# Optimization experiments

Measured on AMD Instinct MI355X. Metric: run time of the kernel, lower is better.

The kernel has to match this reference:

```python
import jax, jax.numpy as jnp
import numpy as np

IN_CH = 512; OUT_CH = 512; NOISE_SIZE = 512; K = 3; A = 0.2
B = 4; H = 32
_G = float(np.sqrt(2.0 / (1.0 + A * A)))                 # leaky_relu gain, a=0.2
CONV_SCALE = _G / float(np.sqrt(IN_CH * K * K))          # equal-lr kaiming scale (fan_in = in_ch*3*3)
MS_SCALE = float(np.sqrt(2.0 / (NOISE_SIZE + IN_CH)))    # equal-lr xavier scale on make_s linear
RGB_SCALE = _G * float(np.sqrt(2.0 / (OUT_CH + 3)))      # equal-lr xavier scale on 1x1 to_rgb


def upsample2x(x):
    # torch F.interpolate(scale_factor=2, mode='bilinear', align_corners=False)
    b, c, h, w = x.shape
    return jax.image.resize(x, (b, c, 2 * h, 2 * w), method='bilinear')


def mod_conv(x, style, weight, bias, ms_w, ms_b, w_scale, demodulate, pad):
    # style -> per-sample input-channel scales s: (B, Cin)
    s = style @ (ms_w.T * MS_SCALE) + ms_b
    Wmod = (weight * w_scale)[None] * s[:, None, :, None, None]   # (B, Cout, Cin, k, k)
    if demodulate:
        d = jax.lax.rsqrt(jnp.sum(Wmod * Wmod, axis=(2, 3, 4)) + 1e-8)
        Wmod = Wmod * d[:, :, None, None, None]
    conv1 = lambda xi, wi: jax.lax.conv_general_dilated(
        xi[None], wi, (1, 1), [(pad, pad), (pad, pad)],
        dimension_numbers=('NCHW', 'OIHW', 'NCHW'))[0]
    y = jax.vmap(conv1)(x, Wmod)                                   # per-sample weights == grouped conv
    return y + bias[None, :, None, None]


def lrelu(x):
    return jnp.where(x >= 0, x, A * x)


def setup_inputs() -> dict:
    key = jax.random.key(0)
    ks = jax.random.split(key, 19)
    r = lambda i, shape: jax.random.normal(ks[i], shape, dtype=jnp.float32)
    return {
        'maps': r(0, (B, IN_CH, H, H)),
        'w': r(1, (B, NOISE_SIZE)),
        'rgb': r(2, (B, 3, H, H)),
        'noise0': r(3, (B, 1, 2 * H, 2 * H)),
        'noise1': r(4, (B, 1, 2 * H, 2 * H)),
        'conv0_w': r(5, (OUT_CH, IN_CH, K, K)),
        'conv0_b': 0.1 * r(6, (OUT_CH,)),
        'ms0_w': r(7, (IN_CH, NOISE_SIZE)),
        'ms0_b': jnp.ones((IN_CH,), jnp.float32),
        'ns0': 0.1 * r(8, (OUT_CH,)),
        'conv1_w': r(9, (OUT_CH, OUT_CH, K, K)),
        'conv1_b': 0.1 * r(10, (OUT_CH,)),
        'ms1_w': r(11, (OUT_CH, NOISE_SIZE)),
        'ms1_b': jnp.ones((OUT_CH,), jnp.float32),
        'ns1': 0.1 * r(12, (OUT_CH,)),
        'rgb_w': r(13, (3, OUT_CH, 1, 1)),
        'rgb_b': 0.1 * r(14, (3,)),
        'msr_w': r(15, (OUT_CH, NOISE_SIZE)),
        'msr_b': jnp.ones((OUT_CH,), jnp.float32),
    }


def reference(maps, w, rgb, noise0, noise1,
              conv0_w, conv0_b, ms0_w, ms0_b, ns0,
              conv1_w, conv1_b, ms1_w, ms1_b, ns1,
              rgb_w, rgb_b, msr_w, msr_b):
    # upsample branch (upsample=True)
    rgb = upsample2x(rgb)
    maps = upsample2x(maps)
    # layer 0: modulated conv -> noise -> leaky relu
    h = mod_conv(maps, w, conv0_w, conv0_b, ms0_w, ms0_b, CONV_SCALE, True, 1)
    h = lrelu(h + ns0[None, :, None, None] * noise0)
    # layer 1
    h = mod_conv(h, w, conv1_w, conv1_b, ms1_w, ms1_b, CONV_SCALE, True, 1)
    h = lrelu(h + ns1[None, :, None, None] * noise1)
    # to_rgb: 1x1 modulated conv, no demodulation
    rgb_out = rgb + mod_conv(h, w, rgb_w, rgb_b, msr_w, msr_b, RGB_SCALE, False, 0)
    return (rgb_out, h)
```

## Files before the change

kernel.cpp:

```cpp
#include <hip/hip_runtime.h>
#include <stdint.h>


#define BATCH 4
#define CH 512
#define NPP 4356
#define HOUT_OFF 49152

static constexpr double G_GAIN = 1.3867504905630728;
static constexpr float CONV_SCALE_F = (float)(G_GAIN / 67.88225099390857);
static constexpr float MS_SCALE_F = 0.044194173824159216f;
static constexpr float RGB_SCALE_F = (float)(G_GAIN * 1.4142135623730951 / 22.693611435820433);

typedef __attribute__((ext_vector_type(8))) short short8;
typedef __attribute__((ext_vector_type(4))) float floatx4;

#define OFF_FLAG   0
#define OFF_S0     256
#define OFF_S1     (OFF_S0 + 8192)
#define OFF_SR     (OFF_S1 + 8192)
#define OFF_D0     (OFF_SR + 8192)
#define OFF_D1     (OFF_D0 + 8192)
#define OFF_B0F    (OFF_D1 + 8192)
#define OFF_B1F    (OFF_B0F + 2048)
#define OFF_NS0F   (OFF_B1F + 2048)
#define OFF_NS1F   (OFF_NS0F + 2048)
#define OFF_RGBBF  (OFF_NS1F + 2048)
#define OFF_WMODR  (OFF_RGBBF + 256)
#define OFF_N0F    (OFF_WMODR + 24576)
#define OFF_N1F    (OFF_N0F + 65536)
#define OFF_WT0    (OFF_N1F + 65536)
#define WT_BYTES   4718592
#define OFF_WT1    (OFF_WT0 + WT_BYTES)
#define OFF_XP0    (OFF_WT1 + WT_BYTES)
#define XP_BYTES   17842176
#define OFF_XP1    (OFF_XP0 + XP_BYTES)

__device__ __forceinline__ float bf2f(unsigned short u) {
  return __uint_as_float(((unsigned int)u) << 16);
}
__device__ __forceinline__ unsigned short f2bf(float f) {
  unsigned int x = __float_as_uint(f);
  unsigned int r = x + 0x7FFFu + ((x >> 16) & 1u);
  return (unsigned short)(r >> 16);
}
__device__ __forceinline__ float ldin(const void* p, long i, int bf) {
  if (bf) return bf2f(((const unsigned short*)p)[i]);
  return ((const float*)p)[i];
}
__device__ __forceinline__ void async_ld16(const void* g, void* l) {
  __builtin_amdgcn_global_load_lds(
      (const __attribute__((address_space(1))) unsigned int*)g,
      (__attribute__((address_space(3))) unsigned int*)l, 16, 0, 0);
}
__device__ __forceinline__ void upw(int o, int n_in, int& lo, int& hi, float& wlo) {
  int k = o >> 1;
  if (o & 1) { lo = k; hi = k + 1; if (hi > n_in - 1) hi = n_in - 1; wlo = 0.75f; }
  else       { lo = k - 1; if (lo < 0) lo = 0; hi = k; wlo = 0.25f; }
}

__global__ void k_flag(const unsigned int* msb, int* flag) {
  if (threadIdx.x == 0 && blockIdx.x == 0)
    *flag = (msb[0] == 0x3F803F80u) ? 1 : 0;
}

__global__ void k_zero(unsigned short* Xp) {
  const int idx = blockIdx.x * 256 + threadIdx.x;
  const int plane = idx / 132;
  const int rem = idx - plane * 132;
  const int row65 = rem >= 66;
  const int col = rem - (row65 ? 66 : 0);
  const short8 z = {0, 0, 0, 0, 0, 0, 0, 0};
  *(short8*)&Xp[((long)plane * NPP + (row65 ? 65 : 0) * 66 + col) * 8] = z;
}

__global__ void k_styles(const void* w, const void* msw0, const void* msb0,
                         const void* msw1, const void* msb1,
                         const void* mswr, const void* msbr,
                         float* s0, float* s1, float* sr, const int* flagp) {
  const int bf = *flagp;
  const int mat = blockIdx.x >> 7, chunk = blockIdx.x & 127;
  const int wv = threadIdx.x >> 6, lane = threadIdx.x & 63;
  const int i = chunk * 4 + wv;
  const void* msw; const void* msb; float* out;
  if (mat == 0)      { msw = msw0; msb = msb0; out = s0; }
  else if (mat == 1) { msw = msw1; msb = msb1; out = s1; }
  else               { msw = mswr; msb = msbr; out = sr; }
  float a[4] = {0.f, 0.f, 0.f, 0.f};
  const int n0 = lane * 8;
  if (bf) {
    short8 m8 = *(const short8*)((const unsigned short*)msw + (long)i * 512 + n0);
    for (int b = 0; b < 4; ++b) {
      short8 w8 = *(const short8*)((const unsigned short*)w + b * 512 + n0);
      float s = 0.f;
      for (int e = 0; e < 8; ++e)
        s += bf2f((unsigned short)m8[e]) * bf2f((unsigned short)w8[e]);
      a[b] = s;
    }
  } else {
    const float* mrow = (const float*)msw + (long)i * 512 + n0;
    float4 m0v = *(const float4*)mrow, m1v = *(const float4*)(mrow + 4);
    for (int b = 0; b < 4; ++b) {
      const float* wr = (const float*)w + b * 512 + n0;
      float4 w0v = *(const float4*)wr, w1v = *(const float4*)(wr + 4);
      a[b] = m0v.x * w0v.x + m0v.y * w0v.y + m0v.z * w0v.z + m0v.w * w0v.w +
             m1v.x * w1v.x + m1v.y * w1v.y + m1v.z * w1v.z + m1v.w * w1v.w;
    }
  }
  for (int off = 1; off < 64; off <<= 1)
    for (int b = 0; b < 4; ++b) a[b] += __shfl_xor(a[b], off, 64);
  if (lane == 0) {
    const float mb = ldin(msb, i, bf);
    for (int b = 0; b < 4; ++b) out[b * 512 + i] = a[b] * MS_SCALE_F + mb;
  }
}

__global__ void k_convert(const void* b0, const void* b1, const void* nv0, const void* nv1,
                          const void* rb, const void* rw, const void* noise0, const void* noise1,
                          float* ob0, float* ob1, float* ons0, float* ons1, float* orb,
                          float* owmr, float* on0, float* on1,
                          const float* sr, const int* flagp) {
  const int bf = *flagp;
  const int t = blockIdx.x * blockDim.x + threadIdx.x;
  const int stride = gridDim.x * blockDim.x;
  if (t < 512) {
    ob0[t] = ldin(b0, t, bf); ob1[t] = ldin(b1, t, bf);
    ons0[t] = ldin(nv0, t, bf); ons1[t] = ldin(nv1, t, bf);
  }
  if (t < 3) orb[t] = ldin(rb, t, bf);
  for (int i = t; i < 16384; i += stride) {
    on0[i] = ldin(noise0, i, bf);
    on1[i] = ldin(noise1, i, bf);
  }
  for (int i = t; i < 4 * 3 * 512; i += stride) {
    int b = i / 1536; int r = i - b * 1536; int c = r >> 9; int ci = r & 511;
    owmr[i] = RGB_SCALE_F * ldin(rw, c * 512 + ci, bf) * sr[b * 512 + ci];
  }
}

__global__ void k_wtd(const void* w0, const void* w1, const float* s0, const float* s1,
                      unsigned short* Wt0, unsigned short* Wt1,
                      float* S0, float* S1, const int* flagp) {
  const int bf = *flagp;
  const int l = blockIdx.x >> 9, co = blockIdx.x & 511;
  const void* w = l ? w1 : w0;
  const float* s = l ? s1 : s0;
  unsigned short* Wt = l ? Wt1 : Wt0;
  float* S = l ? S1 : S0;
  float part[4] = {0.f, 0.f, 0.f, 0.f};
  for (int h = 0; h < 2; ++h) {
    const int ci = threadIdx.x + h * 256;
    const int kb = ci >> 5, q = (ci >> 3) & 3, j = ci & 7;
    const long rbase = ((long)co * 512 + ci) * 9;
    float wsq = 0.f;
    for (int t = 0; t < 9; ++t) {
      float v = ldin(w, rbase + t, bf);
      wsq += v * v;
      Wt[((((long)t * 16 + kb) * 4 + q) * 512 + co) * 8 + j] = f2bf(v);
    }
    for (int b = 0; b < 4; ++b) {
      float sv = s[b * 512 + ci];
      part[b] += sv * sv * wsq;
    }
  }
  __shared__ float red[256 * 4];
  for (int b = 0; b < 4; ++b) red[threadIdx.x * 4 + b] = part[b];
  __syncthreads();
  for (int off = 128; off > 0; off >>= 1) {
    if (threadIdx.x < off)
      for (int b = 0; b < 4; ++b)
        red[threadIdx.x * 4 + b] += red[(threadIdx.x + off) * 4 + b];
    __syncthreads();
  }
  if (threadIdx.x < 4) S[threadIdx.x * 512 + co] = red[threadIdx.x];
}

__global__ void k_upt(const void* maps, const float* s0, unsigned short* Xp0,
                      const int* flagp) {
  const int bf = *flagp;
  const int t = blockIdx.x, kb = blockIdx.y, b = blockIdx.z;
  __shared__ float lds[32][4][32];
  {
    const int ciq = threadIdx.x >> 5;
    const int x = threadIdx.x & 31;
    for (int cc = 0; cc < 4; ++cc) {
      const int ci = cc * 8 + ciq;
      const long cbase = ((long)(b * 512 + kb * 32 + ci)) << 10;
      for (int r = 0; r < 4; ++r) {
        int ir = 2 * t - 1 + r;
        ir = ir < 0 ? 0 : (ir > 31 ? 31 : ir);
        lds[ci][r][x] = ldin(maps, cbase + ir * 32 + x, bf);
      }
    }
  }
  __syncthreads();
  const int q = threadIdx.x >> 6, px = threadIdx.x & 63;
  int xlo, xhi; float wx;
  upw(px, 32, xlo, xhi, wx);
  float sv[8];
  for (int jj = 0; jj < 8; ++jj) sv[jj] = s0[b * 512 + kb * 32 + q * 8 + jj];
  for (int y = 0; y < 4; ++y) {
    const int yg = 4 * t + y;
    int ylo, yhi; float wy;
    upw(yg, 32, ylo, yhi, wy);
    const int rlo = ylo - (2 * t - 1), rhi = yhi - (2 * t - 1);
    short8 pk;
    for (int jj = 0; jj < 8; ++jj) {
      const int ci = q * 8 + jj;
      float vlo = wx * lds[ci][rlo][xlo] + (1.f - wx) * lds[ci][rlo][xhi];
      float vhi = wx * lds[ci][rhi][xlo] + (1.f - wx) * lds[ci][rhi][xhi];
      float v = (wy * vlo + (1.f - wy) * vhi) * sv[jj];
      pk[jj] = (short)f2bf(v);
    }
    *(short8*)&Xp0[((((long)b * 16 + kb) * 4 + q) * NPP + (yg + 1) * 66 + (px + 1)) * 8] = pk;
  }
}

#define MFMA16 __builtin_amdgcn_mfma_f32_16x16x32_bf16
template <int LAYER>
__global__ __launch_bounds__(256, 2) void k_conv(
    const unsigned short* __restrict__ Wt,
    const unsigned short* Xp,
    const float* __restrict__ Ssum,
    const float* __restrict__ bias,
    const float* __restrict__ nsc,
    const float* __restrict__ noise,
    const float* __restrict__ snext,
    unsigned short* XpOut,
    void* dout,
    const int* __restrict__ flagp) {
  __shared__ __align__(16) unsigned short Bl[8192];
  const int idx = blockIdx.x;
  const int mt = idx & 3, b = (idx >> 2) & 3, nt = idx >> 4;
  const int m0 = mt << 7, y0 = nt << 1;
  const int lane = threadIdx.x & 63, wv = threadIdx.x >> 6;
  const int wm = wv >> 1, wn = wv & 1;
  const int q = lane >> 4, l15 = lane & 15;

  const floatx4 vz = {0.f, 0.f, 0.f, 0.f};
  floatx4 c00 = vz, c01 = vz, c02 = vz, c03 = vz;
  floatx4 c10 = vz, c11 = vz, c12 = vz, c13 = vz;
  floatx4 c20 = vz, c21 = vz, c22 = vz, c23 = vz;
  floatx4 c30 = vz, c31 = vz, c32 = vz, c33 = vz;

  const unsigned short* Wbase = Wt + ((long)q * 512 + m0 + wm * 64 + l15) * 8;

  auto issueB2 = [&](int kb, int r0) {
    for (int r = 0; r < 2; ++r) {
      const int row = r0 + r;
      const unsigned short* src =
          Xp + ((((long)b * 16 + kb) * 4 + wv) * NPP + (long)(y0 + row) * 66 + 1 + lane) * 8;
      async_ld16(src, &Bl[((row * 4 + wv) * 64) * 8]);
    }
  };

  issueB2(0, 0);

  const short8 z8 = {0, 0, 0, 0, 0, 0, 0, 0};
#pragma unroll 1
  for (int kb = 0; kb < 16; ++kb) {
#pragma unroll 1
    for (int ky = 0; ky < 3; ++ky) {
      short8 a_[3][4];
#pragma unroll
      for (int kx = 0; kx < 3; ++kx) {
        const unsigned short* ap = Wbase + ((long)((ky * 3 + kx) * 16 + kb) * 4) * 512 * 8;
#pragma unroll
        for (int i = 0; i < 4; ++i)
          a_[kx][i] = *(const short8*)(ap + i * 128);
      }
      __syncthreads();
      if (ky == 0) issueB2(kb, 2);
      else if (ky == 2) issueB2(kb + 1 == 16 ? 0 : kb + 1, 0);
      const int sq = ((wn + ky) * 4 + q) * 64;
#define TAPC(KX)                                                               \
  {                                                                            \
    short8 aa0 = a_[KX][0], aa1 = a_[KX][1], aa2 = a_[KX][2], aa3 = a_[KX][3]; \
    short8 bb0, bb1, bb2, bb3;                                                 \
    {                                                                          \
      int p = 0 * 16 + l15 + (KX);                                             \
      int pc = p < 1 ? 0 : p - 1;                                              \
      bb0 = *(const short8*)&Bl[(sq + pc) * 8];                                \
      if ((KX) == 0) bb0 = (p == 0) ? z8 : bb0;                                \
    }                                                                          \
    bb1 = *(const short8*)&Bl[(sq + 1 * 16 + l15 + (KX)-1) * 8];               \
    bb2 = *(const short8*)&Bl[(sq + 2 * 16 + l15 + (KX)-1) * 8];               \
    {                                                                          \
      int p = 3 * 16 + l15 + (KX);                                             \
      int pc = p > 64 ? 63 : p - 1;                                            \
      bb3 = *(const short8*)&Bl[(sq + pc) * 8];                                \
      if ((KX) == 2) bb3 = (p == 65) ? z8 : bb3;                               \
    }                                                                          \
    c00 = MFMA16(aa0, bb0, c00, 0, 0, 0); c01 = MFMA16(aa0, bb1, c01, 0, 0, 0);\
    c02 = MFMA16(aa0, bb2, c02, 0, 0, 0); c03 = MFMA16(aa0, bb3, c03, 0, 0, 0);\
    c10 = MFMA16(aa1, bb0, c10, 0, 0, 0); c11 = MFMA16(aa1, bb1, c11, 0, 0, 0);\
    c12 = MFMA16(aa1, bb2, c12, 0, 0, 0); c13 = MFMA16(aa1, bb3, c13, 0, 0, 0);\
    c20 = MFMA16(aa2, bb0, c20, 0, 0, 0); c21 = MFMA16(aa2, bb1, c21, 0, 0, 0);\
    c22 = MFMA16(aa2, bb2, c22, 0, 0, 0); c23 = MFMA16(aa2, bb3, c23, 0, 0, 0);\
    c30 = MFMA16(aa3, bb0, c30, 0, 0, 0); c31 = MFMA16(aa3, bb1, c31, 0, 0, 0);\
    c32 = MFMA16(aa3, bb2, c32, 0, 0, 0); c33 = MFMA16(aa3, bb3, c33, 0, 0, 0);\
  }
      TAPC(0)
      TAPC(1)
      TAPC(2)
#undef TAPC
    }
  }

  floatx4 accv[4][4] = {{c00, c01, c02, c03}, {c10, c11, c12, c13},
                        {c20, c21, c22, c23}, {c30, c31, c32, c33}};
  const int bfflag = *flagp;
  const int coB = m0 + (wm << 6) + ((lane >> 4) << 2);
  const int xB = lane & 15;
  const int y = y0 + wn;
  for (int i = 0; i < 4; ++i) {
    const int co = coB + (i << 4);
    float Ds[4], bi[4], nv[4], sx[4];
    for (int r = 0; r < 4; ++r) {
      float Sv = Ssum[b * 512 + co + r];
      Ds[r] = CONV_SCALE_F * rsqrtf(CONV_SCALE_F * CONV_SCALE_F * Sv + 1e-8f);
      bi[r] = bias[co + r];
      nv[r] = nsc[co + r];
      sx[r] = (LAYER == 0) ? snext[b * 512 + co + r] : 0.f;
    }
    for (int j = 0; j < 4; ++j) {
      const int x = (j << 4) + xB;
      const int p = (y << 6) + x;
      const float nz = noise[b * 4096 + p];
      if (LAYER == 0) {
        unsigned long long pk = 0ull;
        for (int r = 0; r < 4; ++r) {
          float v = accv[i][j][r] * Ds[r] + bi[r] + nv[r] * nz;
          v = (v >= 0.f) ? v : 0.2f * v;
          pk |= (unsigned long long)f2bf(v * sx[r]) << (16 * r);
        }
        const int pp = (y + 1) * 66 + (x + 1);
        const long o = ((((long)b * 16 + (co >> 5)) * 4 + ((co >> 3) & 3)) * NPP + pp) * 8 + (co & 7);
        *(unsigned long long*)(XpOut + o) = pk;
      } else {
        for (int r = 0; r < 4; ++r) {
          float v = accv[i][j][r] * Ds[r] + bi[r] + nv[r] * nz;
          v = (v >= 0.f) ? v : 0.2f * v;
          const long o = (((long)(b * 512 + co + r)) << 12) + p;
          if (bfflag) ((unsigned short*)dout)[HOUT_OFF + o] = f2bf(v);
          else        ((float*)dout)[HOUT_OFF + o] = v;
        }
      }
    }
  }
}

__global__ void k_rgb(const void* rgb_in, const float* wmodr, const float* rgbb,
                      void* dout, const int* flagp) {
  const int bf = *flagp;
  const int b = blockIdx.y, p0 = blockIdx.x * 64;
  const int px = threadIdx.x & 63, g = threadIdx.x >> 6;
  const char* hbytes = (const char*)dout + (long)HOUT_OFF * (bf ? 2 : 4);
  float a0 = 0.f, a1 = 0.f, a2 = 0.f;
  const float* wm = wmodr + b * 1536;
  for (int ci = g * 128; ci < g * 128 + 128; ++ci) {
    const long o = (((long)(b * 512 + ci)) << 12) + p0 + px;
    const float hv = bf ? bf2f(((const unsigned short*)hbytes)[o])
                        : ((const float*)hbytes)[o];
    a0 += wm[ci] * hv;
    a1 += wm[512 + ci] * hv;
    a2 += wm[1024 + ci] * hv;
  }
  __shared__ float red[4][3][64];
  red[g][0][px] = a0; red[g][1][px] = a1; red[g][2][px] = a2;
  __syncthreads();
  if (g == 0) {
    const int p = p0 + px;
    const int y = p >> 6, x = p & 63;
    int ylo, yhi, xlo, xhi; float wy, wx;
    upw(y, 32, ylo, yhi, wy);
    upw(x, 32, xlo, xhi, wx);
    for (int c = 0; c < 3; ++c) {
      float s = red[0][c][px] + red[1][c][px] + red[2][c][px] + red[3][c][px];
      const long base = (long)(b * 3 + c) << 10;
      const float v00 = ldin(rgb_in, base + ylo * 32 + xlo, bf);
      const float v01 = ldin(rgb_in, base + ylo * 32 + xhi, bf);
      const float v10 = ldin(rgb_in, base + yhi * 32 + xlo, bf);
      const float v11 = ldin(rgb_in, base + yhi * 32 + xhi, bf);
      const float up = wy * (wx * v00 + (1.f - wx) * v01) +
                       (1.f - wy) * (wx * v10 + (1.f - wx) * v11);
      const float v = up + s + rgbb[c];
      const long o = ((long)(b * 3 + c) << 12) + p;
      if (bf) ((unsigned short*)dout)[o] = f2bf(v);
      else    ((float*)dout)[o] = v;
    }
  }
}

extern "C" void kernel_launch(void* const* d_in, const int* in_sizes, int n_in,
                              void* d_out, int out_size, void* d_ws, size_t ws_size,
                              hipStream_t stream) {
  char* ws = (char*)d_ws;
  int* flag = (int*)(ws + OFF_FLAG);
  float* s0 = (float*)(ws + OFF_S0);
  float* s1 = (float*)(ws + OFF_S1);
  float* sr = (float*)(ws + OFF_SR);
  float* S0 = (float*)(ws + OFF_D0);
  float* S1 = (float*)(ws + OFF_D1);
  float* b0f = (float*)(ws + OFF_B0F);
  float* b1f = (float*)(ws + OFF_B1F);
  float* ns0f = (float*)(ws + OFF_NS0F);
  float* ns1f = (float*)(ws + OFF_NS1F);
  float* rgbbf = (float*)(ws + OFF_RGBBF);
  float* wmodr = (float*)(ws + OFF_WMODR);
  float* n0f = (float*)(ws + OFF_N0F);
  float* n1f = (float*)(ws + OFF_N1F);
  unsigned short* Wt0 = (unsigned short*)(ws + OFF_WT0);
  unsigned short* Wt1 = (unsigned short*)(ws + OFF_WT1);
  unsigned short* Xp0 = (unsigned short*)(ws + OFF_XP0);
  unsigned short* Xp1 = (unsigned short*)(ws + OFF_XP1);

  k_flag<<<1, 64, 0, stream>>>((const unsigned int*)d_in[8], flag);
  k_zero<<<264, 256, 0, stream>>>(Xp0);
  k_styles<<<384, 256, 0, stream>>>(d_in[1], d_in[7], d_in[8], d_in[12], d_in[13],
                                    d_in[17], d_in[18], s0, s1, sr, flag);
  k_convert<<<64, 256, 0, stream>>>(d_in[6], d_in[11], d_in[9], d_in[14], d_in[16],
                                    d_in[15], d_in[3], d_in[4], b0f, b1f, ns0f, ns1f,
                                    rgbbf, wmodr, n0f, n1f, sr, flag);
  k_wtd<<<1024, 256, 0, stream>>>(d_in[5], d_in[10], s0, s1, Wt0, Wt1, S0, S1, flag);
  k_upt<<<dim3(16, 16, 4), 256, 0, stream>>>(d_in[0], s0, Xp0, flag);
  k_conv<0><<<512, 256, 0, stream>>>(Wt0, Xp0, S0, b0f, ns0f, n0f, s1, Xp1,
                                     d_out, flag);
  k_conv<1><<<512, 256, 0, stream>>>(Wt1, Xp1, S1, b1f, ns1f, n1f, s1, Xp1,
                                     d_out, flag);
  k_rgb<<<dim3(64, 4), 256, 0, stream>>>(d_in[2], wmodr, rgbbf, d_out, flag);
  (void)in_sizes; (void)n_in; (void)out_size; (void)ws_size;
}
```

Baseline: 297.9 us.

## Double-buffer weight fragments in registers and overlap loads with MFMA rounds

Splits the conv main loop into rounds that load the next (kb,ky) weight fragments into a second register buffer while MFMAs consume the current one. The loop is unrolled by two kb steps with ping-pong buffers. It uses a hand-written s_waitcnt vmcnt(12) plus barrier, so the outstanding next-round loads are not waited on. This hides global weight-load latency behind compute, at the cost of more VGPRs and reliance on an exact count of in-flight memory ops.

```diff
diff --git a/kernel.cpp b/kernel.cpp
--- a/kernel.cpp
+++ b/kernel.cpp
@@ -254,28 +254,27 @@
     }
   };
 
-  issueB2(0, 0);
+  short8 aA[3][4], aB[3][4];
+
+#define LOADA(BUF, KB, KY)                                                     \
+  {                                                                            \
+    _Pragma("unroll") for (int kx = 0; kx < 3; ++kx) {                         \
+      const unsigned short* ap =                                               \
+          Wbase + ((long)((((KY) * 3 + kx) * 16) + (KB)) << 14);               \
+      _Pragma("unroll") for (int i = 0; i < 4; ++i)                            \
+          BUF[kx][i] = *(const short8*)(ap + i * 128);                         \
+    }                                                                          \
+  }
+
+#define WAITBAR() \
+  asm volatile("s_waitcnt vmcnt(12) lgkmcnt(0)\n\ts_barrier" ::: "memory")
 
   const short8 z8 = {0, 0, 0, 0, 0, 0, 0, 0};
-#pragma unroll 1
-  for (int kb = 0; kb < 16; ++kb) {
-#pragma unroll 1
-    for (int ky = 0; ky < 3; ++ky) {
-      short8 a_[3][4];
-#pragma unroll
-      for (int kx = 0; kx < 3; ++kx) {
-        const unsigned short* ap = Wbase + ((long)((ky * 3 + kx) * 16 + kb) * 4) * 512 * 8;
-#pragma unroll
-        for (int i = 0; i < 4; ++i)
-          a_[kx][i] = *(const short8*)(ap + i * 128);
-      }
-      __syncthreads();
-      if (ky == 0) issueB2(kb, 2);
-      else if (ky == 2) issueB2(kb + 1 == 16 ? 0 : kb + 1, 0);
-      const int sq = ((wn + ky) * 4 + q) * 64;
-#define TAPC(KX)                                                               \
+
+#define TAPC(BUF, KX)                                                          \
   {                                                                            \
-    short8 aa0 = a_[KX][0], aa1 = a_[KX][1], aa2 = a_[KX][2], aa3 = a_[KX][3]; \
+    short8 aa0 = BUF[KX][0], aa1 = BUF[KX][1], aa2 = BUF[KX][2],               \
+           aa3 = BUF[KX][3];                                                   \
     short8 bb0, bb1, bb2, bb3;                                                 \
     {                                                                          \
       int p = 0 * 16 + l15 + (KX);                                             \
@@ -300,12 +299,37 @@
     c30 = MFMA16(aa3, bb0, c30, 0, 0, 0); c31 = MFMA16(aa3, bb1, c31, 0, 0, 0);\
     c32 = MFMA16(aa3, bb2, c32, 0, 0, 0); c33 = MFMA16(aa3, bb3, c33, 0, 0, 0);\
   }
-      TAPC(0)
-      TAPC(1)
-      TAPC(2)
+
+#define ROUND(CUR, NXT, KY, NKB, NKY, DODMA, DKB, DR0)                         \
+  {                                                                            \
+    LOADA(NXT, NKB, NKY);                                                      \
+    WAITBAR();                                                                 \
+    if (DODMA) issueB2((DKB), (DR0));                                          \
+    const int sq = ((wn + (KY)) * 4 + q) * 64;                                 \
+    TAPC(CUR, 0)                                                               \
+    TAPC(CUR, 1)                                                               \
+    TAPC(CUR, 2)                                                               \
+  }
+
+  issueB2(0, 0);
+  LOADA(aA, 0, 0);
+
+#pragma unroll 1
+  for (int it = 0; it < 8; ++it) {
+    const int kb = it * 2;
+    const int kb1 = kb + 1;
+    const int kb2 = (kb + 2) & 15;
+    ROUND(aA, aB, 0, kb, 1, 1, kb, 2);
+    ROUND(aB, aA, 1, kb, 2, 0, 0, 0);
+    ROUND(aA, aB, 2, kb1, 0, 1, kb1, 0);
+    ROUND(aB, aA, 0, kb1, 1, 1, kb1, 2);
+    ROUND(aA, aB, 1, kb1, 2, 0, 0, 0);
+    ROUND(aB, aA, 2, kb2, 0, 1, kb2, 0);
+  }
+#undef ROUND
 #undef TAPC
-    }
-  }
+#undef WAITBAR
+#undef LOADA
 
   floatx4 accv[4][4] = {{c00, c01, c02, c03}, {c10, c11, c12, c13},
                         {c20, c21, c22, c23}, {c30, c31, c32, c33}};
```

New measurement: 292.8 us. About the same (-1.7%).

## Shrink conv tile to one output row per block with double-buffered input rows

Applied to the files above, without the earlier changes.

The modulated conv kernel now gives each block one output row instead of two, and each wave 32 output channels instead of 64. This halves the accumulator registers and doubles the grid to 1024 blocks, with launch bounds raised to 4 blocks per CU for higher occupancy. Input rows are loaded three at a time into a double-buffered LDS region, so the next channel block is prefetched while the current one is computed, and the three kx taps are read with shifted LDS offsets. In exchange, weight tiles are reused across fewer pixels, so global weight traffic per FLOP rises, and each block loads three input rows to produce only one.

```diff
diff --git a/kernel.cpp b/kernel.cpp
--- a/kernel.cpp
+++ b/kernel.cpp
@@ -218,7 +218,7 @@
 
 #define MFMA16 __builtin_amdgcn_mfma_f32_16x16x32_bf16
 template <int LAYER>
-__global__ __launch_bounds__(256, 2) void k_conv(
+__global__ __launch_bounds__(256, 4) void k_conv(
     const unsigned short* __restrict__ Wt,
     const unsigned short* Xp,
     const float* __restrict__ Ssum,
@@ -229,91 +229,109 @@
     unsigned short* XpOut,
     void* dout,
     const int* __restrict__ flagp) {
-  __shared__ __align__(16) unsigned short Bl[8192];
+  __shared__ __align__(16) unsigned short Bl[16384];
   const int idx = blockIdx.x;
   const int mt = idx & 3, b = (idx >> 2) & 3, nt = idx >> 4;
-  const int m0 = mt << 7, y0 = nt << 1;
-  const int lane = threadIdx.x & 63, wv = threadIdx.x >> 6;
-  const int wm = wv >> 1, wn = wv & 1;
+  const int m0 = mt << 7, y0 = nt;
+  const int lane = threadIdx.x & 63, wm = threadIdx.x >> 6;
   const int q = lane >> 4, l15 = lane & 15;
 
   const floatx4 vz = {0.f, 0.f, 0.f, 0.f};
   floatx4 c00 = vz, c01 = vz, c02 = vz, c03 = vz;
   floatx4 c10 = vz, c11 = vz, c12 = vz, c13 = vz;
-  floatx4 c20 = vz, c21 = vz, c22 = vz, c23 = vz;
-  floatx4 c30 = vz, c31 = vz, c32 = vz, c33 = vz;
-
-  const unsigned short* Wbase = Wt + ((long)q * 512 + m0 + wm * 64 + l15) * 8;
-
-  auto issueB2 = [&](int kb, int r0) {
-    for (int r = 0; r < 2; ++r) {
-      const int row = r0 + r;
+
+  const int aoff = (((q << 9) + m0 + (wm << 5) + l15) << 3);
+
+  const int vB   = (q << 9) + (l15 << 3);
+  const int vBm1 = (q << 9) + ((l15 == 0 ? 0 : l15 - 1) << 3);
+  const int vBp1 = (q << 9) + ((l15 == 15 ? 15 : l15 + 1) << 3);
+  const bool e0 = (l15 == 0);
+  const bool e15 = (l15 == 15);
+
+  auto issueB3 = [&](int kbn, int par) {
+    for (int r = 0; r < 3; ++r) {
       const unsigned short* src =
-          Xp + ((((long)b * 16 + kb) * 4 + wv) * NPP + (long)(y0 + row) * 66 + 1 + lane) * 8;
-      async_ld16(src, &Bl[((row * 4 + wv) * 64) * 8]);
+          Xp + ((((long)b * 16 + kbn) * 4 + wm) * NPP + (long)(y0 + r) * 66 + 1 + lane) * 8;
+      async_ld16(src, &Bl[(par << 13) + (r << 11) + (wm << 9)]);
     }
   };
 
-  issueB2(0, 0);
-
   const short8 z8 = {0, 0, 0, 0, 0, 0, 0, 0};
+
+#define RND(KY, PAR, KB, DODMA, DKB, DPAR)                                     \
+  {                                                                            \
+    short8 a00, a01, a10, a11, a20, a21;                                       \
+    {                                                                          \
+      const unsigned short* rp0 = Wt + ((long)(((KY)*3 + 0) * 16 + (KB)) << 14); \
+      a00 = *(const short8*)(rp0 + aoff);                                      \
+      a01 = *(const short8*)(rp0 + aoff + 128);                                \
+      const unsigned short* rp1 = Wt + ((long)(((KY)*3 + 1) * 16 + (KB)) << 14); \
+      a10 = *(const short8*)(rp1 + aoff);                                      \
+      a11 = *(const short8*)(rp1 + aoff + 128);                                \
+      const unsigned short* rp2 = Wt + ((long)(((KY)*3 + 2) * 16 + (KB)) << 14); \
+      a20 = *(const short8*)(rp2 + aoff);                                      \
+      a21 = *(const short8*)(rp2 + aoff + 128);                                \
+    }                                                                          \
+    __syncthreads();                                                           \
+    if (DODMA) issueB3((DKB), (DPAR));                                         \
+    const int bo = (PAR) * 8192 + (KY) * 2048;                                 \
+                                                                   \
+    {                                                                          \
+      short8 b0 = *(const short8*)&Bl[vBm1 + bo];                              \
+      short8 b1 = *(const short8*)&Bl[vB + bo + 120];                          \
+      short8 b2 = *(const short8*)&Bl[vB + bo + 248];                          \
+      short8 b3 = *(const short8*)&Bl[vB + bo + 376];                          \
+      b0 = e0 ? z8 : b0;                                                       \
+      c00 = MFMA16(a00, b0, c00, 0, 0, 0); c01 = MFMA16(a00, b1, c01, 0, 0, 0);\
+      c02 = MFMA16(a00, b2, c02, 0, 0, 0); c03 = MFMA16(a00, b3, c03, 0, 0, 0);\
+      c10 = MFMA16(a01, b0, c10, 0, 0, 0); c11 = MFMA16(a01, b1, c11, 0, 0, 0);\
+      c12 = MFMA16(a01, b2, c12, 0, 0, 0); c13 = MFMA16(a01, b3, c13, 0, 0, 0);\
+    }                                                                          \
+                                                                   \
+    {                                                                          \
+      short8 b0 = *(const short8*)&Bl[vB + bo];                                \
+      short8 b1 = *(const short8*)&Bl[vB + bo + 128];                          \
+      short8 b2 = *(const short8*)&Bl[vB + bo + 256];                          \
+      short8 b3 = *(const short8*)&Bl[vB + bo + 384];                          \
+      c00 = MFMA16(a10, b0, c00, 0, 0, 0); c01 = MFMA16(a10, b1, c01, 0, 0, 0);\
+      c02 = MFMA16(a10, b2, c02, 0, 0, 0); c03 = MFMA16(a10, b3, c03, 0, 0, 0);\
+      c10 = MFMA16(a11, b0, c10, 0, 0, 0); c11 = MFMA16(a11, b1, c11, 0, 0, 0);\
+      c12 = MFMA16(a11, b2, c12, 0, 0, 0); c13 = MFMA16(a11, b3, c13, 0, 0, 0);\
+    }                                                                          \
+                                                                   \
+    {                                                                          \
+      short8 b0 = *(const short8*)&Bl[vB + bo + 8];                            \
+      short8 b1 = *(const short8*)&Bl[vB + bo + 136];                          \
+      short8 b2 = *(const short8*)&Bl[vB + bo + 264];                          \
+      short8 b3 = *(const short8*)&Bl[vBp1 + bo + 384];                        \
+      b3 = e15 ? z8 : b3;                                                      \
+      c00 = MFMA16(a20, b0, c00, 0, 0, 0); c01 = MFMA16(a20, b1, c01, 0, 0, 0);\
+      c02 = MFMA16(a20, b2, c02, 0, 0, 0); c03 = MFMA16(a20, b3, c03, 0, 0, 0);\
+      c10 = MFMA16(a21, b0, c10, 0, 0, 0); c11 = MFMA16(a21, b1, c11, 0, 0, 0);\
+      c12 = MFMA16(a21, b2, c12, 0, 0, 0); c13 = MFMA16(a21, b3, c13, 0, 0, 0);\
+    }                                                                          \
+  }
+
+  issueB3(0, 0);
+
 #pragma unroll 1
-  for (int kb = 0; kb < 16; ++kb) {
-#pragma unroll 1
-    for (int ky = 0; ky < 3; ++ky) {
-      short8 a_[3][4];
-#pragma unroll
-      for (int kx = 0; kx < 3; ++kx) {
-        const unsigned short* ap = Wbase + ((long)((ky * 3 + kx) * 16 + kb) * 4) * 512 * 8;
-#pragma unroll
-        for (int i = 0; i < 4; ++i)
-          a_[kx][i] = *(const short8*)(ap + i * 128);
-      }
-      __syncthreads();
-      if (ky == 0) issueB2(kb, 2);
-      else if (ky == 2) issueB2(kb + 1 == 16 ? 0 : kb + 1, 0);
-      const int sq = ((wn + ky) * 4 + q) * 64;
-#define TAPC(KX)                                                               \
-  {                                                                            \
-    short8 aa0 = a_[KX][0], aa1 = a_[KX][1], aa2 = a_[KX][2], aa3 = a_[KX][3]; \
-    short8 bb0, bb1, bb2, bb3;                                                 \
-    {                                                                          \
-      int p = 0 * 16 + l15 + (KX);                                             \
-      int pc = p < 1 ? 0 : p - 1;                                              \
-      bb0 = *(const short8*)&Bl[(sq + pc) * 8];                                \
-      if ((KX) == 0) bb0 = (p == 0) ? z8 : bb0;                                \
-    }                                                                          \
-    bb1 = *(const short8*)&Bl[(sq + 1 * 16 + l15 + (KX)-1) * 8];               \
-    bb2 = *(const short8*)&Bl[(sq + 2 * 16 + l15 + (KX)-1) * 8];               \
-    {                                                                          \
-      int p = 3 * 16 + l15 + (KX);                                             \
-      int pc = p > 64 ? 63 : p - 1;                                            \
-      bb3 = *(const short8*)&Bl[(sq + pc) * 8];                                \
-      if ((KX) == 2) bb3 = (p == 65) ? z8 : bb3;                               \
-    }                                                                          \
-    c00 = MFMA16(aa0, bb0, c00, 0, 0, 0); c01 = MFMA16(aa0, bb1, c01, 0, 0, 0);\
-    c02 = MFMA16(aa0, bb2, c02, 0, 0, 0); c03 = MFMA16(aa0, bb3, c03, 0, 0, 0);\
-    c10 = MFMA16(aa1, bb0, c10, 0, 0, 0); c11 = MFMA16(aa1, bb1, c11, 0, 0, 0);\
-    c12 = MFMA16(aa1, bb2, c12, 0, 0, 0); c13 = MFMA16(aa1, bb3, c13, 0, 0, 0);\
-    c20 = MFMA16(aa2, bb0, c20, 0, 0, 0); c21 = MFMA16(aa2, bb1, c21, 0, 0, 0);\
-    c22 = MFMA16(aa2, bb2, c22, 0, 0, 0); c23 = MFMA16(aa2, bb3, c23, 0, 0, 0);\
-    c30 = MFMA16(aa3, bb0, c30, 0, 0, 0); c31 = MFMA16(aa3, bb1, c31, 0, 0, 0);\
-    c32 = MFMA16(aa3, bb2, c32, 0, 0, 0); c33 = MFMA16(aa3, bb3, c33, 0, 0, 0);\
-  }
-      TAPC(0)
-      TAPC(1)
-      TAPC(2)
-#undef TAPC
-    }
-  }
-
-  floatx4 accv[4][4] = {{c00, c01, c02, c03}, {c10, c11, c12, c13},
-                        {c20, c21, c22, c23}, {c30, c31, c32, c33}};
+  for (int it = 0; it < 8; ++it) {
+    const int kb = it * 2;
+    RND(0, 0, kb, 1, kb + 1, 1)
+    RND(1, 0, kb, 0, 0, 0)
+    RND(2, 0, kb, 0, 0, 0)
+    RND(0, 1, kb + 1, 1, (kb + 2) & 15, 0)
+    RND(1, 1, kb + 1, 0, 0, 0)
+    RND(2, 1, kb + 1, 0, 0, 0)
+  }
+#undef RND
+
+  floatx4 accv[2][4] = {{c00, c01, c02, c03}, {c10, c11, c12, c13}};
   const int bfflag = *flagp;
-  const int coB = m0 + (wm << 6) + ((lane >> 4) << 2);
+  const int coB = m0 + (wm << 5) + ((lane >> 4) << 2);
   const int xB = lane & 15;
-  const int y = y0 + wn;
-  for (int i = 0; i < 4; ++i) {
+  const int y = y0;
+  for (int i = 0; i < 2; ++i) {
     const int co = coB + (i << 4);
     float Ds[4], bi[4], nv[4], sx[4];
     for (int r = 0; r < 4; ++r) {
@@ -424,10 +442,10 @@
                                     rgbbf, wmodr, n0f, n1f, sr, flag);
   k_wtd<<<1024, 256, 0, stream>>>(d_in[5], d_in[10], s0, s1, Wt0, Wt1, S0, S1, flag);
   k_upt<<<dim3(16, 16, 4), 256, 0, stream>>>(d_in[0], s0, Xp0, flag);
-  k_conv<0><<<512, 256, 0, stream>>>(Wt0, Xp0, S0, b0f, ns0f, n0f, s1, Xp1,
-                                     d_out, flag);
-  k_conv<1><<<512, 256, 0, stream>>>(Wt1, Xp1, S1, b1f, ns1f, n1f, s1, Xp1,
-                                     d_out, flag);
+  k_conv<0><<<1024, 256, 0, stream>>>(Wt0, Xp0, S0, b0f, ns0f, n0f, s1, Xp1,
+                                      d_out, flag);
+  k_conv<1><<<1024, 256, 0, stream>>>(Wt1, Xp1, S1, b1f, ns1f, n1f, s1, Xp1,
+                                      d_out, flag);
   k_rgb<<<dim3(64, 4), 256, 0, stream>>>(d_in[2], wmodr, rgbbf, d_out, flag);
   (void)in_sizes; (void)n_in; (void)out_size; (void)ws_size;
 }
```

Result: slower. 320.7 us (+7.7%).

## Stage conv weights in LDS with double buffering and fuse preprocessing kernels

Applied to the files above, without the earlier changes.

The conv kernel now loads weight tiles into LDS asynchronously with a ping-pong buffer, so the next (kb, ky) slice is prefetched while MFMAs run on the current one. Before, every wave read its weights straight from global memory into registers. The flag, zero, styles and convert kernels are merged into one k_pre launch, and each kernel reads the bf16 flag directly from the input to cut launch count. The rgb modulated weights are now computed inside k_rgb instead of being precomputed, which adds per-iteration weight loads there. LDS use grows from 16KB to 64KB per block, which may lower occupancy.

```diff
diff --git a/kernel.cpp b/kernel.cpp
--- a/kernel.cpp
+++ b/kernel.cpp
@@ -15,7 +15,6 @@
 typedef __attribute__((ext_vector_type(8))) short short8;
 typedef __attribute__((ext_vector_type(4))) float floatx4;
 
-#define OFF_FLAG   0
 #define OFF_S0     256
 #define OFF_S1     (OFF_S0 + 8192)
 #define OFF_SR     (OFF_S1 + 8192)
@@ -25,9 +24,7 @@
 #define OFF_B1F    (OFF_B0F + 2048)
 #define OFF_NS0F   (OFF_B1F + 2048)
 #define OFF_NS1F   (OFF_NS0F + 2048)
-#define OFF_RGBBF  (OFF_NS1F + 2048)
-#define OFF_WMODR  (OFF_RGBBF + 256)
-#define OFF_N0F    (OFF_WMODR + 24576)
+#define OFF_N0F    (OFF_NS1F + 2048)
 #define OFF_N1F    (OFF_N0F + 65536)
 #define OFF_WT0    (OFF_N1F + 65536)
 #define WT_BYTES   4718592
@@ -48,6 +45,9 @@
   if (bf) return bf2f(((const unsigned short*)p)[i]);
   return ((const float*)p)[i];
 }
+__device__ __forceinline__ int bfflag_of(const void* msb) {
+  return ((const unsigned int*)msb)[0] == 0x3F803F80u ? 1 : 0;
+}
 __device__ __forceinline__ void async_ld16(const void* g, void* l) {
   __builtin_amdgcn_global_load_lds(
       (const __attribute__((address_space(1))) unsigned int*)g,
@@ -59,89 +59,77 @@
   else       { lo = k - 1; if (lo < 0) lo = 0; hi = k; wlo = 0.25f; }
 }
 
-__global__ void k_flag(const unsigned int* msb, int* flag) {
-  if (threadIdx.x == 0 && blockIdx.x == 0)
-    *flag = (msb[0] == 0x3F803F80u) ? 1 : 0;
-}
-
-__global__ void k_zero(unsigned short* Xp) {
-  const int idx = blockIdx.x * 256 + threadIdx.x;
-  const int plane = idx / 132;
-  const int rem = idx - plane * 132;
-  const int row65 = rem >= 66;
-  const int col = rem - (row65 ? 66 : 0);
-  const short8 z = {0, 0, 0, 0, 0, 0, 0, 0};
-  *(short8*)&Xp[((long)plane * NPP + (row65 ? 65 : 0) * 66 + col) * 8] = z;
-}
-
-__global__ void k_styles(const void* w, const void* msw0, const void* msb0,
-                         const void* msw1, const void* msb1,
-                         const void* mswr, const void* msbr,
-                         float* s0, float* s1, float* sr, const int* flagp) {
-  const int bf = *flagp;
-  const int mat = blockIdx.x >> 7, chunk = blockIdx.x & 127;
-  const int wv = threadIdx.x >> 6, lane = threadIdx.x & 63;
-  const int i = chunk * 4 + wv;
-  const void* msw; const void* msb; float* out;
-  if (mat == 0)      { msw = msw0; msb = msb0; out = s0; }
-  else if (mat == 1) { msw = msw1; msb = msb1; out = s1; }
-  else               { msw = mswr; msb = msbr; out = sr; }
-  float a[4] = {0.f, 0.f, 0.f, 0.f};
-  const int n0 = lane * 8;
-  if (bf) {
-    short8 m8 = *(const short8*)((const unsigned short*)msw + (long)i * 512 + n0);
-    for (int b = 0; b < 4; ++b) {
-      short8 w8 = *(const short8*)((const unsigned short*)w + b * 512 + n0);
-      float s = 0.f;
-      for (int e = 0; e < 8; ++e)
-        s += bf2f((unsigned short)m8[e]) * bf2f((unsigned short)w8[e]);
-      a[b] = s;
-    }
-  } else {
-    const float* mrow = (const float*)msw + (long)i * 512 + n0;
-    float4 m0v = *(const float4*)mrow, m1v = *(const float4*)(mrow + 4);
-    for (int b = 0; b < 4; ++b) {
-      const float* wr = (const float*)w + b * 512 + n0;
-      float4 w0v = *(const float4*)wr, w1v = *(const float4*)(wr + 4);
-      a[b] = m0v.x * w0v.x + m0v.y * w0v.y + m0v.z * w0v.z + m0v.w * w0v.w +
-             m1v.x * w1v.x + m1v.y * w1v.y + m1v.z * w1v.z + m1v.w * w1v.w;
-    }
-  }
-  for (int off = 1; off < 64; off <<= 1)
-    for (int b = 0; b < 4; ++b) a[b] += __shfl_xor(a[b], off, 64);
-  if (lane == 0) {
-    const float mb = ldin(msb, i, bf);
-    for (int b = 0; b < 4; ++b) out[b * 512 + i] = a[b] * MS_SCALE_F + mb;
-  }
-}
-
-__global__ void k_convert(const void* b0, const void* b1, const void* nv0, const void* nv1,
-                          const void* rb, const void* rw, const void* noise0, const void* noise1,
-                          float* ob0, float* ob1, float* ons0, float* ons1, float* orb,
-                          float* owmr, float* on0, float* on1,
-                          const float* sr, const int* flagp) {
-  const int bf = *flagp;
-  const int t = blockIdx.x * blockDim.x + threadIdx.x;
-  const int stride = gridDim.x * blockDim.x;
+__global__ void k_pre(const void* w, const void* msw0, const void* msb0,
+                      const void* msw1, const void* msb1,
+                      const void* mswr, const void* msbr,
+                      const void* b0, const void* b1, const void* nv0,
+                      const void* nv1, const void* noise0, const void* noise1,
+                      float* s0, float* s1, float* sr,
+                      float* ob0, float* ob1, float* ons0, float* ons1,
+                      float* on0, float* on1, unsigned short* Xp) {
+  const int bf = bfflag_of(msb0);
+  const int bid = blockIdx.x;
+  if (bid < 264) {
+    const int idx = bid * 256 + threadIdx.x;
+    const int plane = idx / 132;
+    const int rem = idx - plane * 132;
+    const int row65 = rem >= 66;
+    const int col = rem - (row65 ? 66 : 0);
+    const short8 z = {0, 0, 0, 0, 0, 0, 0, 0};
+    *(short8*)&Xp[((long)plane * NPP + (row65 ? 65 : 0) * 66 + col) * 8] = z;
+    return;
+  }
+  if (bid < 648) {
+    const int b2 = bid - 264;
+    const int mat = b2 >> 7, chunk = b2 & 127;
+    const int wv = threadIdx.x >> 6, lane = threadIdx.x & 63;
+    const int i = chunk * 4 + wv;
+    const void* msw; const void* msb; float* out;
+    if (mat == 0)      { msw = msw0; msb = msb0; out = s0; }
+    else if (mat == 1) { msw = msw1; msb = msb1; out = s1; }
+    else               { msw = mswr; msb = msbr; out = sr; }
+    float a[4] = {0.f, 0.f, 0.f, 0.f};
+    const int n0 = lane * 8;
+    if (bf) {
+      short8 m8 = *(const short8*)((const unsigned short*)msw + (long)i * 512 + n0);
+      for (int b = 0; b < 4; ++b) {
+        short8 w8 = *(const short8*)((const unsigned short*)w + b * 512 + n0);
+        float s = 0.f;
+        for (int e = 0; e < 8; ++e)
+          s += bf2f((unsigned short)m8[e]) * bf2f((unsigned short)w8[e]);
+        a[b] = s;
+      }
+    } else {
+      const float* mrow = (const float*)msw + (long)i * 512 + n0;
+      float4 m0v = *(const float4*)mrow, m1v = *(const float4*)(mrow + 4);
+      for (int b = 0; b < 4; ++b) {
+        const float* wr = (const float*)w + b * 512 + n0;
+        float4 w0v = *(const float4*)wr, w1v = *(const float4*)(wr + 4);
+        a[b] = m0v.x * w0v.x + m0v.y * w0v.y + m0v.z * w0v.z + m0v.w * w0v.w +
+               m1v.x * w1v.x + m1v.y * w1v.y + m1v.z * w1v.z + m1v.w * w1v.w;
+      }
+    }
+    for (int off = 1; off < 64; off <<= 1)
+      for (int b = 0; b < 4; ++b) a[b] += __shfl_xor(a[b], off, 64);
+    if (lane == 0) {
+      const float mb = ldin(msb, i, bf);
+      for (int b = 0; b < 4; ++b) out[b * 512 + i] = a[b] * MS_SCALE_F + mb;
+    }
+    return;
+  }
+  const int t = (bid - 648) * 256 + threadIdx.x;
   if (t < 512) {
     ob0[t] = ldin(b0, t, bf); ob1[t] = ldin(b1, t, bf);
     ons0[t] = ldin(nv0, t, bf); ons1[t] = ldin(nv1, t, bf);
   }
-  if (t < 3) orb[t] = ldin(rb, t, bf);
-  for (int i = t; i < 16384; i += stride) {
-    on0[i] = ldin(noise0, i, bf);
-    on1[i] = ldin(noise1, i, bf);
-  }
-  for (int i = t; i < 4 * 3 * 512; i += stride) {
-    int b = i / 1536; int r = i - b * 1536; int c = r >> 9; int ci = r & 511;
-    owmr[i] = RGB_SCALE_F * ldin(rw, c * 512 + ci, bf) * sr[b * 512 + ci];
-  }
+  on0[t] = ldin(noise0, t, bf);
+  on1[t] = ldin(noise1, t, bf);
 }
 
 __global__ void k_wtd(const void* w0, const void* w1, const float* s0, const float* s1,
                       unsigned short* Wt0, unsigned short* Wt1,
-                      float* S0, float* S1, const int* flagp) {
-  const int bf = *flagp;
+                      float* S0, float* S1, const void* msb) {
+  const int bf = bfflag_of(msb);
   const int l = blockIdx.x >> 9, co = blockIdx.x & 511;
   const void* w = l ? w1 : w0;
   const float* s = l ? s1 : s0;
@@ -176,8 +164,8 @@
 }
 
 __global__ void k_upt(const void* maps, const float* s0, unsigned short* Xp0,
-                      const int* flagp) {
-  const int bf = *flagp;
+                      const void* msb) {
+  const int bf = bfflag_of(msb);
   const int t = blockIdx.x, kb = blockIdx.y, b = blockIdx.z;
   __shared__ float lds[32][4][32];
   {
@@ -228,8 +216,8 @@
     const float* __restrict__ snext,
     unsigned short* XpOut,
     void* dout,
-    const int* __restrict__ flagp) {
-  __shared__ __align__(16) unsigned short Bl[8192];
+    const void* __restrict__ msb) {
+  __shared__ __align__(16) unsigned short AB[32768];
   const int idx = blockIdx.x;
   const int mt = idx & 3, b = (idx >> 2) & 3, nt = idx >> 4;
   const int m0 = mt << 7, y0 = nt << 1;
@@ -243,73 +231,120 @@
   floatx4 c20 = vz, c21 = vz, c22 = vz, c23 = vz;
   floatx4 c30 = vz, c31 = vz, c32 = vz, c33 = vz;
 
-  const unsigned short* Wbase = Wt + ((long)q * 512 + m0 + wm * 64 + l15) * 8;
+  const int vA = (q << 10) + (wm << 9) + (l15 << 3);
+  const int BB = 24576;
+  const int vB   = BB + (q << 9) + (l15 << 3);
+  const int vBm1 = BB + (q << 9) + ((l15 == 0 ? 0 : l15 - 1) << 3);
+  const int vBp1 = BB + (q << 9) + ((l15 == 15 ? 15 : l15 + 1) << 3);
+  const bool e0 = (l15 == 0), e15 = (l15 == 15);
+  const int c6 = wv * 6;
 
   auto issueB2 = [&](int kb, int r0) {
     for (int r = 0; r < 2; ++r) {
       const int row = r0 + r;
       const unsigned short* src =
           Xp + ((((long)b * 16 + kb) * 4 + wv) * NPP + (long)(y0 + row) * 66 + 1 + lane) * 8;
-      async_ld16(src, &Bl[((row * 4 + wv) * 64) * 8]);
+      async_ld16(src, &AB[BB + ((row * 4 + wv) << 9)]);
     }
   };
-
+  auto issueA = [&](int kb, int ky, int par) {
+#pragma unroll
+    for (int k = 0; k < 6; ++k) {
+      const int c = c6 + k;
+      const int half = c & 1, chunk = c >> 1;
+      const int kx = chunk >> 2, qq = chunk & 3;
+      const unsigned short* src =
+          Wt + ((long)(((ky * 3 + kx) * 16 + kb) * 4 + qq) << 12) +
+          ((m0 + half * 64 + lane) << 3);
+      async_ld16(src, &AB[par * 12288 + chunk * 1024 + half * 512]);
+    }
+  };
+
+  const short8 z8 = {0, 0, 0, 0, 0, 0, 0, 0};
+
+#define RND(KY, PA, KB, NKB, NKY, NPA, DOB, DKB, DR0)                          \
+  {                                                                            \
+    __syncthreads();                                                           \
+    issueA((NKB), (NKY), (NPA));                                               \
+    if (DOB) issueB2((DKB), (DR0));                                            \
+    const int ab = (PA) * 12288 + vA;                                          \
+    short8 a00 = *(const short8*)&AB[ab];                                      \
+    short8 a01 = *(const short8*)&AB[ab + 128];                                \
+    short8 a02 = *(const short8*)&AB[ab + 256];                                \
+    short8 a03 = *(const short8*)&AB[ab + 384];                                \
+    short8 a10 = *(const short8*)&AB[ab + 4096];                               \
+    short8 a11 = *(const short8*)&AB[ab + 4224];                               \
+    short8 a12 = *(const short8*)&AB[ab + 4352];                               \
+    short8 a13 = *(const short8*)&AB[ab + 4480];                               \
+    short8 a20 = *(const short8*)&AB[ab + 8192];                               \
+    short8 a21 = *(const short8*)&AB[ab + 8320];                               \
+    short8 a22 = *(const short8*)&AB[ab + 8448];                               \
+    short8 a23 = *(const short8*)&AB[ab + 8576];                               \
+    const int bo = ((wn + (KY)) << 11);                                        \
+    {                                                              \
+      short8 b0 = *(const short8*)&AB[vBm1 + bo];                              \
+      short8 b1 = *(const short8*)&AB[vB + bo + 120];                          \
+      short8 b2 = *(const short8*)&AB[vB + bo + 248];                          \
+      short8 b3 = *(const short8*)&AB[vB + bo + 376];                          \
+      b0 = e0 ? z8 : b0;                                                       \
+      c00 = MFMA16(a00, b0, c00, 0, 0, 0); c01 = MFMA16(a00, b1, c01, 0, 0, 0);\
+      c02 = MFMA16(a00, b2, c02, 0, 0, 0); c03 = MFMA16(a00, b3, c03, 0, 0, 0);\
+      c10 = MFMA16(a01, b0, c10, 0, 0, 0); c11 = MFMA16(a01, b1, c11, 0, 0, 0);\
+      c12 = MFMA16(a01, b2, c12, 0, 0, 0); c13 = MFMA16(a01, b3, c13, 0, 0, 0);\
+      c20 = MFMA16(a02, b0, c20, 0, 0, 0); c21 = MFMA16(a02, b1, c21, 0, 0, 0);\
+      c22 = MFMA16(a02, b2, c22, 0, 0, 0); c23 = MFMA16(a02, b3, c23, 0, 0, 0);\
+      c30 = MFMA16(a03, b0, c30, 0, 0, 0); c31 = MFMA16(a03, b1, c31, 0, 0, 0);\
+      c32 = MFMA16(a03, b2, c32, 0, 0, 0); c33 = MFMA16(a03, b3, c33, 0, 0, 0);\
+    }                                                                          \
+    {                                                              \
+      short8 b0 = *(const short8*)&AB[vB + bo];                                \
+      short8 b1 = *(const short8*)&AB[vB + bo + 128];                          \
+      short8 b2 = *(const short8*)&AB[vB + bo + 256];                          \
+      short8 b3 = *(const short8*)&AB[vB + bo + 384];                          \
+      c00 = MFMA16(a10, b0, c00, 0, 0, 0); c01 = MFMA16(a10, b1, c01, 0, 0, 0);\
+      c02 = MFMA16(a10, b2, c02, 0, 0, 0); c03 = MFMA16(a10, b3, c03, 0, 0, 0);\
+      c10 = MFMA16(a11, b0, c10, 0, 0, 0); c11 = MFMA16(a11, b1, c11, 0, 0, 0);\
+      c12 = MFMA16(a11, b2, c12, 0, 0, 0); c13 = MFMA16(a11, b3, c13, 0, 0, 0);\
+      c20 = MFMA16(a12, b0, c20, 0, 0, 0); c21 = MFMA16(a12, b1, c21, 0, 0, 0);\
+      c22 = MFMA16(a12, b2, c22, 0, 0, 0); c23 = MFMA16(a12, b3, c23, 0, 0, 0);\
+      c30 = MFMA16(a13, b0, c30, 0, 0, 0); c31 = MFMA16(a13, b1, c31, 0, 0, 0);\
+      c32 = MFMA16(a13, b2, c32, 0, 0, 0); c33 = MFMA16(a13, b3, c33, 0, 0, 0);\
+    }                                                                          \
+    {                                                              \
+      short8 b0 = *(const short8*)&AB[vB + bo + 8];                            \
+      short8 b1 = *(const short8*)&AB[vB + bo + 136];                          \
+      short8 b2 = *(const short8*)&AB[vB + bo + 264];                          \
+      short8 b3 = *(const short8*)&AB[vBp1 + bo + 384];                        \
+      b3 = e15 ? z8 : b3;                                                      \
+      c00 = MFMA16(a20, b0, c00, 0, 0, 0); c01 = MFMA16(a20, b1, c01, 0, 0, 0);\
+      c02 = MFMA16(a20, b2, c02, 0, 0, 0); c03 = MFMA16(a20, b3, c03, 0, 0, 0);\
+      c10 = MFMA16(a21, b0, c10, 0, 0, 0); c11 = MFMA16(a21, b1, c11, 0, 0, 0);\
+      c12 = MFMA16(a21, b2, c12, 0, 0, 0); c13 = MFMA16(a21, b3, c13, 0, 0, 0);\
+      c20 = MFMA16(a22, b0, c20, 0, 0, 0); c21 = MFMA16(a22, b1, c21, 0, 0, 0);\
+      c22 = MFMA16(a22, b2, c22, 0, 0, 0); c23 = MFMA16(a22, b3, c23, 0, 0, 0);\
+      c30 = MFMA16(a23, b0, c30, 0, 0, 0); c31 = MFMA16(a23, b1, c31, 0, 0, 0);\
+      c32 = MFMA16(a23, b2, c32, 0, 0, 0); c33 = MFMA16(a23, b3, c33, 0, 0, 0);\
+    }                                                                          \
+  }
+
+  issueA(0, 0, 0);
   issueB2(0, 0);
 
-  const short8 z8 = {0, 0, 0, 0, 0, 0, 0, 0};
 #pragma unroll 1
-  for (int kb = 0; kb < 16; ++kb) {
-#pragma unroll 1
-    for (int ky = 0; ky < 3; ++ky) {
-      short8 a_[3][4];
-#pragma unroll
-      for (int kx = 0; kx < 3; ++kx) {
-        const unsigned short* ap = Wbase + ((long)((ky * 3 + kx) * 16 + kb) * 4) * 512 * 8;
-#pragma unroll
-        for (int i = 0; i < 4; ++i)
-          a_[kx][i] = *(const short8*)(ap + i * 128);
-      }
-      __syncthreads();
-      if (ky == 0) issueB2(kb, 2);
-      else if (ky == 2) issueB2(kb + 1 == 16 ? 0 : kb + 1, 0);
-      const int sq = ((wn + ky) * 4 + q) * 64;
-#define TAPC(KX)                                                               \
-  {                                                                            \
-    short8 aa0 = a_[KX][0], aa1 = a_[KX][1], aa2 = a_[KX][2], aa3 = a_[KX][3]; \
-    short8 bb0, bb1, bb2, bb3;                                                 \
-    {                                                                          \
-      int p = 0 * 16 + l15 + (KX);                                             \
-      int pc = p < 1 ? 0 : p - 1;                                              \
-      bb0 = *(const short8*)&Bl[(sq + pc) * 8];                                \
-      if ((KX) == 0) bb0 = (p == 0) ? z8 : bb0;                                \
-    }                                                                          \
-    bb1 = *(const short8*)&Bl[(sq + 1 * 16 + l15 + (KX)-1) * 8];               \
-    bb2 = *(const short8*)&Bl[(sq + 2 * 16 + l15 + (KX)-1) * 8];               \
-    {                                                                          \
-      int p = 3 * 16 + l15 + (KX);                                             \
-      int pc = p > 64 ? 63 : p - 1;                                            \
-      bb3 = *(const short8*)&Bl[(sq + pc) * 8];                                \
-      if ((KX) == 2) bb3 = (p == 65) ? z8 : bb3;                               \
-    }                                                                          \
-    c00 = MFMA16(aa0, bb0, c00, 0, 0, 0); c01 = MFMA16(aa0, bb1, c01, 0, 0, 0);\
-    c02 = MFMA16(aa0, bb2, c02, 0, 0, 0); c03 = MFMA16(aa0, bb3, c03, 0, 0, 0);\
-    c10 = MFMA16(aa1, bb0, c10, 0, 0, 0); c11 = MFMA16(aa1, bb1, c11, 0, 0, 0);\
-    c12 = MFMA16(aa1, bb2, c12, 0, 0, 0); c13 = MFMA16(aa1, bb3, c13, 0, 0, 0);\
-    c20 = MFMA16(aa2, bb0, c20, 0, 0, 0); c21 = MFMA16(aa2, bb1, c21, 0, 0, 0);\
-    c22 = MFMA16(aa2, bb2, c22, 0, 0, 0); c23 = MFMA16(aa2, bb3, c23, 0, 0, 0);\
-    c30 = MFMA16(aa3, bb0, c30, 0, 0, 0); c31 = MFMA16(aa3, bb1, c31, 0, 0, 0);\
-    c32 = MFMA16(aa3, bb2, c32, 0, 0, 0); c33 = MFMA16(aa3, bb3, c33, 0, 0, 0);\
-  }
-      TAPC(0)
-      TAPC(1)
-      TAPC(2)
-#undef TAPC
-    }
-  }
+  for (int it = 0; it < 8; ++it) {
+    const int kb = it * 2, kb1 = kb + 1, kb2 = (kb + 2) & 15;
+    RND(0, 0, kb,  kb,  1, 1, 1, kb,  2)
+    RND(1, 1, kb,  kb,  2, 0, 0, 0,  0)
+    RND(2, 0, kb,  kb1, 0, 1, 1, kb1, 0)
+    RND(0, 1, kb1, kb1, 1, 0, 1, kb1, 2)
+    RND(1, 0, kb1, kb1, 2, 1, 0, 0,  0)
+    RND(2, 1, kb1, kb2, 0, 0, 1, kb2, 0)
+  }
+#undef RND
 
   floatx4 accv[4][4] = {{c00, c01, c02, c03}, {c10, c11, c12, c13},
                         {c20, c21, c22, c23}, {c30, c31, c32, c33}};
-  const int bfflag = *flagp;
+  const int bfflag = bfflag_of(msb);
   const int coB = m0 + (wm << 6) + ((lane >> 4) << 2);
   const int xB = lane & 15;
   const int y = y0 + wn;
@@ -350,21 +385,22 @@
   }
 }
 
-__global__ void k_rgb(const void* rgb_in, const float* wmodr, const float* rgbb,
-                      void* dout, const int* flagp) {
-  const int bf = *flagp;
+__global__ void k_rgb(const void* rgb_in, const void* rw, const void* rb,
+                      const float* sr, void* dout, const void* msb) {
+  const int bf = bfflag_of(msb);
   const int b = blockIdx.y, p0 = blockIdx.x * 64;
   const int px = threadIdx.x & 63, g = threadIdx.x >> 6;
   const char* hbytes = (const char*)dout + (long)HOUT_OFF * (bf ? 2 : 4);
+  const float* srb = sr + b * 512;
   float a0 = 0.f, a1 = 0.f, a2 = 0.f;
-  const float* wm = wmodr + b * 1536;
   for (int ci = g * 128; ci < g * 128 + 128; ++ci) {
     const long o = (((long)(b * 512 + ci)) << 12) + p0 + px;
     const float hv = bf ? bf2f(((const unsigned short*)hbytes)[o])
                         : ((const float*)hbytes)[o];
-    a0 += wm[ci] * hv;
-    a1 += wm[512 + ci] * hv;
-    a2 += wm[1024 + ci] * hv;
+    const float sh = srb[ci] * hv;
+    a0 += RGB_SCALE_F * ldin(rw, ci, bf) * sh;
+    a1 += RGB_SCALE_F * ldin(rw, 512 + ci, bf) * sh;
+    a2 += RGB_SCALE_F * ldin(rw, 1024 + ci, bf) * sh;
   }
   __shared__ float red[4][3][64];
   red[g][0][px] = a0; red[g][1][px] = a1; red[g][2][px] = a2;
@@ -384,7 +420,7 @@
       const float v11 = ldin(rgb_in, base + yhi * 32 + xhi, bf);
       const float up = wy * (wx * v00 + (1.f - wx) * v01) +
                        (1.f - wy) * (wx * v10 + (1.f - wx) * v11);
-      const float v = up + s + rgbb[c];
+      const float v = up + s + ldin(rb, c, bf);
       const long o = ((long)(b * 3 + c) << 12) + p;
       if (bf) ((unsigned short*)dout)[o] = f2bf(v);
       else    ((float*)dout)[o] = v;
@@ -396,7 +432,6 @@
                               void* d_out, int out_size, void* d_ws, size_t ws_size,
                               hipStream_t stream) {
   char* ws = (char*)d_ws;
-  int* flag = (int*)(ws + OFF_FLAG);
   float* s0 = (float*)(ws + OFF_S0);
   float* s1 = (float*)(ws + OFF_S1);
   float* sr = (float*)(ws + OFF_SR);
@@ -406,8 +441,6 @@
   float* b1f = (float*)(ws + OFF_B1F);
   float* ns0f = (float*)(ws + OFF_NS0F);
   float* ns1f = (float*)(ws + OFF_NS1F);
-  float* rgbbf = (float*)(ws + OFF_RGBBF);
-  float* wmodr = (float*)(ws + OFF_WMODR);
   float* n0f = (float*)(ws + OFF_N0F);
   float* n1f = (float*)(ws + OFF_N1F);
   unsigned short* Wt0 = (unsigned short*)(ws + OFF_WT0);
@@ -415,19 +448,18 @@
   unsigned short* Xp0 = (unsigned short*)(ws + OFF_XP0);
   unsigned short* Xp1 = (unsigned short*)(ws + OFF_XP1);
 
-  k_flag<<<1, 64, 0, stream>>>((const unsigned int*)d_in[8], flag);
-  k_zero<<<264, 256, 0, stream>>>(Xp0);
-  k_styles<<<384, 256, 0, stream>>>(d_in[1], d_in[7], d_in[8], d_in[12], d_in[13],
-                                    d_in[17], d_in[18], s0, s1, sr, flag);
-  k_convert<<<64, 256, 0, stream>>>(d_in[6], d_in[11], d_in[9], d_in[14], d_in[16],
-                                    d_in[15], d_in[3], d_in[4], b0f, b1f, ns0f, ns1f,
-                                    rgbbf, wmodr, n0f, n1f, sr, flag);
-  k_wtd<<<1024, 256, 0, stream>>>(d_in[5], d_in[10], s0, s1, Wt0, Wt1, S0, S1, flag);
-  k_upt<<<dim3(16, 16, 4), 256, 0, stream>>>(d_in[0], s0, Xp0, flag);
+  k_pre<<<712, 256, 0, stream>>>(d_in[1], d_in[7], d_in[8], d_in[12], d_in[13],
+                                 d_in[17], d_in[18], d_in[6], d_in[11], d_in[9],
+                                 d_in[14], d_in[3], d_in[4],
+                                 s0, s1, sr, b0f, b1f, ns0f, ns1f, n0f, n1f, Xp0);
+  k_wtd<<<1024, 256, 0, stream>>>(d_in[5], d_in[10], s0, s1, Wt0, Wt1, S0, S1,
+                                  d_in[8]);
+  k_upt<<<dim3(16, 16, 4), 256, 0, stream>>>(d_in[0], s0, Xp0, d_in[8]);
   k_conv<0><<<512, 256, 0, stream>>>(Wt0, Xp0, S0, b0f, ns0f, n0f, s1, Xp1,
-                                     d_out, flag);
+                                     d_out, d_in[8]);
   k_conv<1><<<512, 256, 0, stream>>>(Wt1, Xp1, S1, b1f, ns1f, n1f, s1, Xp1,
-                                     d_out, flag);
-  k_rgb<<<dim3(64, 4), 256, 0, stream>>>(d_in[2], wmodr, rgbbf, d_out, flag);
+                                     d_out, d_in[8]);
+  k_rgb<<<dim3(64, 4), 256, 0, stream>>>(d_in[2], d_in[15], d_in[16], sr, d_out,
+                                         d_in[8]);
   (void)in_sizes; (void)n_in; (void)out_size; (void)ws_size;
 }
```

Result: slower. 305.0 us (+2.4%).
